# Kernel tuning notes

Hardware: AMD Instinct MI355X
Metric: run time of the kernel (lower is better)

Reference implementation:

```python
import jax, jax.numpy as jnp
import numpy as np

# tcnn HashGrid config from ntc_conf
L = 16            # n_levels
T = 1 << 15       # 2**log2_hashmap_size entries per level
F = 4             # n_features_per_level
BASE = 16.0       # base_resolution
N_PTS = 1_000_000
PRIMES = jnp.array([1, 2654435761, 805459861], dtype=jnp.uint32)  # tcnn spatial hash primes
OFFS = np.array([[(c >> 2) & 1, (c >> 1) & 1, c & 1] for c in range(8)], dtype=np.uint32)  # 8 cube corners


def hash_encode(x, table):
    """Multi-resolution hash grid encoding. x: [N,3] in [0,1], table: [L,T,F] -> [N, L*F]."""
    N = x.shape[0]
    scales = BASE * (2.0 ** jnp.arange(L, dtype=jnp.float32))        # [L]
    pos = x[:, None, :] * scales[None, :, None]                      # [N,L,3]
    p0 = jnp.floor(pos)
    frac = pos - p0                                                  # trilinear weights source
    p0u = p0.astype(jnp.uint32)
    flat_table = table.reshape(L * T, F)
    level_off = (jnp.arange(L, dtype=jnp.uint32) * jnp.uint32(T))[None, :]  # [1,L]
    acc = jnp.zeros((N, L, F), dtype=table.dtype)
    for c in range(8):  # fixed 8 corners -> keeps peak memory at [N,L,F] per corner
        off = jnp.asarray(OFFS[c])                                   # [3] uint32
        corner = p0u + off                                           # [N,L,3]
        h = corner * PRIMES                                          # uint32 wraparound mul
        idx = (h[..., 0] ^ h[..., 1] ^ h[..., 2]) & jnp.uint32(T - 1)  # [N,L]
        feats = flat_table[(idx + level_off).astype(jnp.int32)]      # gather [N,L,F]
        w = jnp.prod(jnp.where(off.astype(bool), frac, 1.0 - frac), axis=-1)  # [N,L]
        acc = acc + w[..., None] * feats
    return acc.reshape(N, L * F)


def setup_inputs() -> dict:
    key = jax.random.key(0)
    k1, k2, k3, k4, k5 = jax.random.split(key, 5)
    xyz = jax.random.normal(k1, (N_PTS, 3), dtype=jnp.float32)
    xyz_bound_min = -jnp.ones((3,), dtype=jnp.float32)
    xyz_bound_max = jnp.ones((3,), dtype=jnp.float32)
    hash_table = jax.random.normal(k2, (L, T, F), dtype=jnp.float32) * 1e-2  # tcnn-style small init
    w0 = jax.random.normal(k3, (64, 64), dtype=jnp.float32) * (1.0 / 8.0)
    w1 = jax.random.normal(k4, (64, 64), dtype=jnp.float32) * (1.0 / 8.0)
    w2 = jax.random.normal(k5, (64, 8), dtype=jnp.float32) * (1.0 / 8.0)
    return {"xyz": xyz, "xyz_bound_min": xyz_bound_min, "xyz_bound_max": xyz_bound_max,
            "hash_table": hash_table, "w0": w0, "w1": w1, "w2": w2}


def reference(xyz, xyz_bound_min, xyz_bound_max, hash_table, w0, w1, w2):
    contracted = (xyz - xyz_bound_min) / (xyz_bound_max - xyz_bound_min)   # [N,3]
    mask = jnp.all((contracted >= 0.0) & (contracted <= 1.0), axis=1)      # [N]
    # Evaluate on all points (clamped) and mask the writes -- equivalent to the
    # original compaction (contracted[mask]) + scatter-back, jit-friendly shapes.
    xin = jnp.clip(contracted, 0.0, 1.0)
    enc = hash_encode(xin, hash_table)                                     # [N,64]
    h = jax.nn.relu(enc @ w0)
    h = jax.nn.relu(h @ w1)
    resi = h @ w2                                                          # [N,8]
    d_xyz = jnp.where(mask[:, None], resi[:, :3], 0.0)
    ident_rot = jnp.array([1.0, 0.0, 0.0, 0.0], dtype=resi.dtype)
    d_rot = jnp.where(mask[:, None], resi[:, 3:7], ident_rot)
    return mask, d_xyz, d_rot
```

## Files before the change

### kernel.cpp

```cpp
#include <hip/hip_runtime.h>
#include <hip/hip_bf16.h>


#define LVL 16
#define TSZ 32768
#define PR1 2654435761u
#define PR2 805459861u

typedef __attribute__((ext_vector_type(8))) short bf16x8;
typedef __attribute__((ext_vector_type(4))) float f32x4;
typedef __attribute__((ext_vector_type(2))) float f32x2;
typedef __attribute__((ext_vector_type(4))) unsigned short u16x4;

__device__ __forceinline__ unsigned short f2bf(float f) {
    return __builtin_bit_cast(unsigned short, __float2bfloat16(f));
}

__device__ __forceinline__ unsigned f32x4_to_fp8x4(float f0, float f1, float f2, float f3) {
#if __has_builtin(__builtin_amdgcn_cvt_pk_fp8_f32)
    int u = 0;
    u = __builtin_amdgcn_cvt_pk_fp8_f32(f0, f1, u, false);
    u = __builtin_amdgcn_cvt_pk_fp8_f32(f2, f3, u, true);
    return (unsigned)u;
#else
    float ff[4] = { f0, f1, f2, f3 };
    unsigned u = 0;
    for (int k = 0; k < 4; ++k) {
        const float v = ff[k];
        const unsigned s = v < 0.f ? 1u : 0u;
        float av = fabsf(v);
        unsigned b;
        if (av < 6.103515625e-05f) {
            b = 0u;
        } else if (av < 0.015625f) {
            b = (unsigned)rintf(av * 512.f);
        } else {
            int e; float m = frexpf(av, &e);
            unsigned E = (unsigned)(e - 1 + 7);
            unsigned q = (unsigned)rintf(m * 16.f);
            if (q == 16u) { q = 8u; ++E; }
            b = (E << 3) | (q - 8u);
        }
        u |= ((s << 7) | b) << (8 * k);
    }
    return u;
#endif
}

__device__ __forceinline__ void fp8x4_to_f32(unsigned r, float f[4]) {
#if __has_builtin(__builtin_amdgcn_cvt_pk_f32_fp8)
    const f32x2 lo = __builtin_amdgcn_cvt_pk_f32_fp8((int)r, false);
    const f32x2 hi = __builtin_amdgcn_cvt_pk_f32_fp8((int)r, true);
    f[0] = lo[0]; f[1] = lo[1]; f[2] = hi[0]; f[3] = hi[1];
#else
#pragma unroll
    for (int k = 0; k < 4; ++k) {
        const unsigned b = (r >> (8 * k)) & 0xffu;
        const unsigned s = b >> 7, em = b & 0x7fu, e = em >> 3, m = em & 7u;
        float v;
        if (e) v = __builtin_bit_cast(float, ((e + 120u) << 23) | (m << 20));
        else   v = (float)m * 0.001953125f;
        f[k] = s ? -v : v;
    }
#endif
}

__global__ __launch_bounds__(256) void k_tbl8(const float* __restrict__ t,
                                              unsigned* __restrict__ o, int n4) {
    const int g = blockIdx.x * 256 + threadIdx.x;
    if (g >= n4) return;
    const float4 a = reinterpret_cast<const float4*>(t)[g];
    o[g] = f32x4_to_fp8x4(a.x * 256.f, a.y * 256.f, a.z * 256.f, a.w * 256.f);
}

__global__ void k_wts(const float* __restrict__ w0, const float* __restrict__ w1,
                      const float* __restrict__ w2, unsigned short* __restrict__ wf) {
    const int t = threadIdx.x;
#pragma unroll
    for (int q = 0; q < 16; ++q) {
        const int s = q * 256 + t;
        const int e = s & 7, f = s >> 3;
        const int lnn = f & 63, ntkk = f >> 6;
        const int k = (ntkk & 1) * 32 + (lnn >> 4) * 8 + e;
        const int n = (ntkk >> 1) * 16 + (lnn & 15);
        wf[s]        = f2bf(w0[k * 64 + n]);
        wf[4096 + s] = f2bf(w1[k * 64 + n]);
    }
#pragma unroll
    for (int q = 0; q < 4; ++q) {
        const int s = q * 256 + t;
        const int e = s & 7, f = s >> 3;
        const int lnn = f & 63, kk = f >> 6;
        const int k = kk * 32 + (lnn >> 4) * 8 + e;
        const int n = lnn & 15;
        wf[8192 + s] = (n < 8) ? f2bf(w2[k * 8 + n]) : (unsigned short)0;
    }
}

__global__ __launch_bounds__(1024) void k_enc(
    const float* __restrict__ xyz, const float* __restrict__ bmin, const float* __restrict__ bmax,
    const unsigned* __restrict__ tbl8, float* __restrict__ out,
    unsigned short* __restrict__ enc, int N, int Npad)
{
    __shared__ unsigned tabL[TSZ];

    const int t = threadIdx.x;
    const int base = blockIdx.x * 4096;

    const float bx0 = bmin[0], by0 = bmin[1], bz0 = bmin[2];
    const float ex = bmax[0] - bx0, ey = bmax[1] - by0, ez = bmax[2] - bz0;

    float X[4], Y[4], Z[4];
#pragma unroll
    for (int q = 0; q < 4; ++q) {
        const int p  = base + q * 1024 + t;
        const int pc = p < N ? p : N - 1;
        const float cx = (xyz[3 * pc + 0] - bx0) / ex;
        const float cy = (xyz[3 * pc + 1] - by0) / ey;
        const float cz = (xyz[3 * pc + 2] - bz0) / ez;
        const bool inside = (cx >= 0.f) && (cx <= 1.f) && (cy >= 0.f) && (cy <= 1.f) &&
                            (cz >= 0.f) && (cz <= 1.f);
        if (p < N) out[p] = inside ? 1.f : 0.f;
        X[q] = fminf(fmaxf(cx, 0.f), 1.f);
        Y[q] = fminf(fmaxf(cy, 0.f), 1.f);
        Z[q] = fminf(fmaxf(cz, 0.f), 1.f);
    }

    for (int l = 0; l < LVL; ++l) {
        __syncthreads();
        {
            const uint4* __restrict__ src = reinterpret_cast<const uint4*>(tbl8 + (size_t)l * TSZ);
            uint4* dst = reinterpret_cast<uint4*>(tabL);
#pragma unroll
            for (int j = 0; j < 8; ++j) dst[j * 1024 + t] = src[j * 1024 + t];
        }
        __syncthreads();

        const float scale = 16.f * (float)(1u << l);
#pragma unroll
        for (int q = 0; q < 4; ++q) {
            const float px = X[q] * scale, py = Y[q] * scale, pz = Z[q] * scale;
            const float fx = floorf(px), fy = floorf(py), fz = floorf(pz);
            const float rx = px - fx, ry = py - fy, rz = pz - fz;
            const unsigned ux = (unsigned)fx, uy = (unsigned)fy, uz = (unsigned)fz;
            const unsigned hx[2] = { ux, ux + 1u };
            const unsigned hy[2] = { uy * PR1, uy * PR1 + PR1 };
            const unsigned hz[2] = { uz * PR2, uz * PR2 + PR2 };
            const float    wx[2] = { 1.f - rx, rx };
            const float    wy[2] = { 1.f - ry, ry };
            const float    wz[2] = { (1.f - rz) * (1.f / 256.f), rz * (1.f / 256.f) };

            unsigned r[8];
#pragma unroll
            for (int c = 0; c < 8; ++c)
                r[c] = tabL[(hx[(c >> 2) & 1] ^ hy[(c >> 1) & 1] ^ hz[c & 1]) & (TSZ - 1u)];

            float a0 = 0.f, a1 = 0.f, a2 = 0.f, a3 = 0.f;
#pragma unroll
            for (int c = 0; c < 8; ++c) {
                float f[4];
                fp8x4_to_f32(r[c], f);
                const float w = wx[(c >> 2) & 1] * wy[(c >> 1) & 1] * wz[c & 1];
                a0 = fmaf(w, f[0], a0);
                a1 = fmaf(w, f[1], a1);
                a2 = fmaf(w, f[2], a2);
                a3 = fmaf(w, f[3], a3);
            }

            const int p = base + q * 1024 + t;
            u16x4 v = { f2bf(a0), f2bf(a1), f2bf(a2), f2bf(a3) };
            *reinterpret_cast<u16x4*>(enc + ((size_t)(l >> 1) * Npad + p) * 8 + (l & 1) * 4) = v;
        }
    }
}

__global__ __launch_bounds__(256) void k_mlp(
    const unsigned short* __restrict__ wf, const unsigned short* __restrict__ enc,
    float* __restrict__ out, int N, int Npad)
{
    __shared__ unsigned short hT[8 * 256 * 8];
    __shared__ float resS[256 * 8];

    const int t = threadIdx.x, wv = t >> 6, ln = t & 63;
    const int col = ln & 15, g = ln >> 4;
    const int ptb = blockIdx.x * 256;
    const int i = ptb + t;

    bf16x8 a0[2][4];
#pragma unroll
    for (int kk = 0; kk < 2; ++kk)
#pragma unroll
        for (int mt = 0; mt < 4; ++mt) {
            const size_t pt = (size_t)ptb + wv * 64 + mt * 16 + col;
            a0[kk][mt] = __builtin_nontemporal_load(
                reinterpret_cast<const bf16x8*>(enc + ((size_t)(kk * 4 + g) * Npad + pt) * 8));
        }
    bf16x8 b0[4][2];
#pragma unroll
    for (int nt = 0; nt < 4; ++nt)
#pragma unroll
        for (int kk = 0; kk < 2; ++kk)
            b0[nt][kk] = *reinterpret_cast<const bf16x8*>(wf + ((nt * 2 + kk) * 64 + ln) * 8);

    f32x4 acc[4][4];
#pragma unroll
    for (int mt = 0; mt < 4; ++mt)
#pragma unroll
        for (int nt = 0; nt < 4; ++nt) acc[mt][nt] = (f32x4){0.f, 0.f, 0.f, 0.f};

#pragma unroll
    for (int kk = 0; kk < 2; ++kk)
#pragma unroll
        for (int nt = 0; nt < 4; ++nt)
#pragma unroll
            for (int mt = 0; mt < 4; ++mt)
                acc[mt][nt] = __builtin_amdgcn_mfma_f32_16x16x32_bf16(a0[kk][mt], b0[nt][kk], acc[mt][nt], 0, 0, 0);

#pragma unroll
    for (int mt = 0; mt < 4; ++mt)
#pragma unroll
        for (int nt = 0; nt < 4; ++nt) {
            const int kt = nt * 2 + (col >> 3), j = col & 7;
#pragma unroll
            for (int r = 0; r < 4; ++r)
                hT[kt * 2048 + (wv * 64 + mt * 16 + g * 4 + r) * 8 + j] =
                    f2bf(fmaxf(acc[mt][nt][r], 0.f));
        }

    bf16x8 b1[4][2];
#pragma unroll
    for (int nt = 0; nt < 4; ++nt)
#pragma unroll
        for (int kk = 0; kk < 2; ++kk)
            b1[nt][kk] = *reinterpret_cast<const bf16x8*>(wf + 4096 + ((nt * 2 + kk) * 64 + ln) * 8);

#pragma unroll
    for (int mt = 0; mt < 4; ++mt)
#pragma unroll
        for (int nt = 0; nt < 4; ++nt) acc[mt][nt] = (f32x4){0.f, 0.f, 0.f, 0.f};

#pragma unroll
    for (int kk = 0; kk < 2; ++kk) {
        bf16x8 a[4];
#pragma unroll
        for (int mt = 0; mt < 4; ++mt)
            a[mt] = *reinterpret_cast<bf16x8*>(
                &hT[(kk * 4 + g) * 2048 + (wv * 64 + mt * 16 + col) * 8]);
#pragma unroll
        for (int nt = 0; nt < 4; ++nt)
#pragma unroll
            for (int mt = 0; mt < 4; ++mt)
                acc[mt][nt] = __builtin_amdgcn_mfma_f32_16x16x32_bf16(a[mt], b1[nt][kk], acc[mt][nt], 0, 0, 0);
    }

#pragma unroll
    for (int mt = 0; mt < 4; ++mt)
#pragma unroll
        for (int nt = 0; nt < 4; ++nt) {
            const int kt = nt * 2 + (col >> 3), j = col & 7;
#pragma unroll
            for (int r = 0; r < 4; ++r)
                hT[kt * 2048 + (wv * 64 + mt * 16 + g * 4 + r) * 8 + j] =
                    f2bf(fmaxf(acc[mt][nt][r], 0.f));
        }

    f32x4 acc2[4];
#pragma unroll
    for (int mt = 0; mt < 4; ++mt) acc2[mt] = (f32x4){0.f, 0.f, 0.f, 0.f};

#pragma unroll
    for (int kk = 0; kk < 2; ++kk) {
        const bf16x8 b2 = *reinterpret_cast<const bf16x8*>(wf + 8192 + (kk * 64 + ln) * 8);
        bf16x8 a[4];
#pragma unroll
        for (int mt = 0; mt < 4; ++mt)
            a[mt] = *reinterpret_cast<bf16x8*>(
                &hT[(kk * 4 + g) * 2048 + (wv * 64 + mt * 16 + col) * 8]);
#pragma unroll
        for (int mt = 0; mt < 4; ++mt)
            acc2[mt] = __builtin_amdgcn_mfma_f32_16x16x32_bf16(a[mt], b2, acc2[mt], 0, 0, 0);
    }

    if (col < 8) {
#pragma unroll
        for (int mt = 0; mt < 4; ++mt)
#pragma unroll
            for (int r = 0; r < 4; ++r)
                resS[(wv * 64 + mt * 16 + g * 4 + r) * 8 + col] = acc2[mt][r];
    }
    __syncthreads();

    if (i < N) {
        const bool inside = (out[i] != 0.f);
        const f32x4 lo = *reinterpret_cast<f32x4*>(&resS[t * 8 + 0]);
        const f32x4 hi = *reinterpret_cast<f32x4*>(&resS[t * 8 + 4]);

        float* __restrict__ dxyz = out + N;
        dxyz[3 * i + 0] = inside ? lo.x : 0.f;
        dxyz[3 * i + 1] = inside ? lo.y : 0.f;
        dxyz[3 * i + 2] = inside ? lo.z : 0.f;

        float4* __restrict__ drot = reinterpret_cast<float4*>(out + 4 * (size_t)N);
        drot[i] = inside ? make_float4(lo.w, hi.x, hi.y, hi.z)
                         : make_float4(1.f, 0.f, 0.f, 0.f);
    }
}

__global__ __launch_bounds__(256) void ntc_fused(
    const float* __restrict__ xyz, const float* __restrict__ bmin, const float* __restrict__ bmax,
    const float* __restrict__ table, const float* __restrict__ w0, const float* __restrict__ w1,
    const float* __restrict__ w2, float* __restrict__ out, int N)
{
    __shared__ unsigned short encT[8 * 256 * 8];
    __shared__ unsigned short w0t[64 * 64];
    __shared__ unsigned short w1t[64 * 64];
    __shared__ unsigned short w2t[16 * 64];

    const int t = threadIdx.x, wv = t >> 6, ln = t & 63;
    const int col = ln & 15, g = ln >> 4;

#pragma unroll
    for (int it = 0; it < 16; ++it) {
        const int idx = it * 256 + t;
        const int k = idx >> 6, n = idx & 63;
        w0t[n * 64 + k] = f2bf(w0[idx]);
        w1t[n * 64 + k] = f2bf(w1[idx]);
    }
#pragma unroll
    for (int q = 0; q < 4; ++q) {
        const int idx = t * 4 + q;
        const int n = idx >> 6, k = idx & 63;
        w2t[idx] = (n < 8) ? f2bf(w2[k * 8 + n]) : (unsigned short)0;
    }

    const int i = blockIdx.x * 256 + t;
    const int ic = (i < N) ? i : (N - 1);
    const float bx0 = bmin[0], by0 = bmin[1], bz0 = bmin[2];
    const float ex = bmax[0] - bx0, ey = bmax[1] - by0, ez = bmax[2] - bz0;
    const float cx = (xyz[3 * ic + 0] - bx0) / ex;
    const float cy = (xyz[3 * ic + 1] - by0) / ey;
    const float cz = (xyz[3 * ic + 2] - bz0) / ez;
    const bool inside = (cx >= 0.f) && (cx <= 1.f) && (cy >= 0.f) && (cy <= 1.f) &&
                        (cz >= 0.f) && (cz <= 1.f);
    const float x = fminf(fmaxf(cx, 0.f), 1.f);
    const float y = fminf(fmaxf(cy, 0.f), 1.f);
    const float z = fminf(fmaxf(cz, 0.f), 1.f);
    const float4* __restrict__ tab = reinterpret_cast<const float4*>(table);

    for (int l = 0; l < LVL; ++l) {
        const float scale = 16.f * (float)(1u << l);
        const float px = x * scale, py = y * scale, pz = z * scale;
        const float fx = floorf(px), fy = floorf(py), fz = floorf(pz);
        const float rx = px - fx, ry = py - fy, rz = pz - fz;
        const unsigned ux = (unsigned)fx, uy = (unsigned)fy, uz = (unsigned)fz;
        const unsigned hx[2] = { ux, ux + 1u };
        const unsigned hy[2] = { uy * PR1, (uy + 1u) * PR1 };
        const unsigned hz[2] = { uz * PR2, (uz + 1u) * PR2 };
        const float wx[2] = { 1.f - rx, rx };
        const float wy[2] = { 1.f - ry, ry };
        const float wz[2] = { 1.f - rz, rz };
        float a0 = 0.f, a1 = 0.f, a2 = 0.f, a3 = 0.f;
#pragma unroll
        for (int c = 0; c < 8; ++c) {
            const int ox = (c >> 2) & 1, oy = (c >> 1) & 1, oz = c & 1;
            const unsigned idx = (hx[ox] ^ hy[oy] ^ hz[oz]) & (TSZ - 1u);
            const float4 f4 = tab[l * TSZ + idx];
            const float w = wx[ox] * wy[oy] * wz[oz];
            a0 = fmaf(w, f4.x, a0); a1 = fmaf(w, f4.y, a1);
            a2 = fmaf(w, f4.z, a2); a3 = fmaf(w, f4.w, a3);
        }
        u16x4 v = { f2bf(a0), f2bf(a1), f2bf(a2), f2bf(a3) };
        *reinterpret_cast<u16x4*>(&encT[(l >> 1) * 2048 + t * 8 + (l & 1) * 4]) = v;
    }
    __syncthreads();

    f32x4 acc[4][4];
#pragma unroll
    for (int mt = 0; mt < 4; ++mt)
#pragma unroll
        for (int nt = 0; nt < 4; ++nt) acc[mt][nt] = (f32x4){0.f, 0.f, 0.f, 0.f};
#pragma unroll
    for (int kk = 0; kk < 2; ++kk) {
        bf16x8 a[4];
#pragma unroll
        for (int mt = 0; mt < 4; ++mt)
            a[mt] = *reinterpret_cast<bf16x8*>(&encT[(kk * 4 + g) * 2048 + (wv * 64 + mt * 16 + col) * 8]);
#pragma unroll
        for (int nt = 0; nt < 4; ++nt) {
            bf16x8 b = *reinterpret_cast<bf16x8*>(&w0t[(nt * 16 + col) * 64 + kk * 32 + g * 8]);
#pragma unroll
            for (int mt = 0; mt < 4; ++mt)
                acc[mt][nt] = __builtin_amdgcn_mfma_f32_16x16x32_bf16(a[mt], b, acc[mt][nt], 0, 0, 0);
        }
    }
    __syncthreads();
#pragma unroll
    for (int mt = 0; mt < 4; ++mt)
#pragma unroll
        for (int nt = 0; nt < 4; ++nt) {
            const int kt = nt * 2 + (col >> 3), j = col & 7;
#pragma unroll
            for (int r = 0; r < 4; ++r)
                encT[kt * 2048 + (wv * 64 + mt * 16 + g * 4 + r) * 8 + j] = f2bf(fmaxf(acc[mt][nt][r], 0.f));
        }
    __syncthreads();
#pragma unroll
    for (int mt = 0; mt < 4; ++mt)
#pragma unroll
        for (int nt = 0; nt < 4; ++nt) acc[mt][nt] = (f32x4){0.f, 0.f, 0.f, 0.f};
#pragma unroll
    for (int kk = 0; kk < 2; ++kk) {
        bf16x8 a[4];
#pragma unroll
        for (int mt = 0; mt < 4; ++mt)
            a[mt] = *reinterpret_cast<bf16x8*>(&encT[(kk * 4 + g) * 2048 + (wv * 64 + mt * 16 + col) * 8]);
#pragma unroll
        for (int nt = 0; nt < 4; ++nt) {
            bf16x8 b = *reinterpret_cast<bf16x8*>(&w1t[(nt * 16 + col) * 64 + kk * 32 + g * 8]);
#pragma unroll
            for (int mt = 0; mt < 4; ++mt)
                acc[mt][nt] = __builtin_amdgcn_mfma_f32_16x16x32_bf16(a[mt], b, acc[mt][nt], 0, 0, 0);
        }
    }
    __syncthreads();
#pragma unroll
    for (int mt = 0; mt < 4; ++mt)
#pragma unroll
        for (int nt = 0; nt < 4; ++nt) {
            const int kt = nt * 2 + (col >> 3), j = col & 7;
#pragma unroll
            for (int r = 0; r < 4; ++r)
                encT[kt * 2048 + (wv * 64 + mt * 16 + g * 4 + r) * 8 + j] = f2bf(fmaxf(acc[mt][nt][r], 0.f));
        }
    __syncthreads();
    f32x4 acc2[4];
#pragma unroll
    for (int mt = 0; mt < 4; ++mt) acc2[mt] = (f32x4){0.f, 0.f, 0.f, 0.f};
#pragma unroll
    for (int kk = 0; kk < 2; ++kk) {
        bf16x8 a[4];
#pragma unroll
        for (int mt = 0; mt < 4; ++mt)
            a[mt] = *reinterpret_cast<bf16x8*>(&encT[(kk * 4 + g) * 2048 + (wv * 64 + mt * 16 + col) * 8]);
        bf16x8 b = *reinterpret_cast<bf16x8*>(&w2t[col * 64 + kk * 32 + g * 8]);
#pragma unroll
        for (int mt = 0; mt < 4; ++mt)
            acc2[mt] = __builtin_amdgcn_mfma_f32_16x16x32_bf16(a[mt], b, acc2[mt], 0, 0, 0);
    }
    __syncthreads();
    float* res = reinterpret_cast<float*>(encT);
    if (col < 8) {
#pragma unroll
        for (int mt = 0; mt < 4; ++mt)
#pragma unroll
            for (int r = 0; r < 4; ++r)
                res[(wv * 64 + mt * 16 + g * 4 + r) * 8 + col] = acc2[mt][r];
    }
    __syncthreads();
    if (i < N) {
        const f32x4 lo = *reinterpret_cast<f32x4*>(&res[t * 8 + 0]);
        const f32x4 hi = *reinterpret_cast<f32x4*>(&res[t * 8 + 4]);
        out[i] = inside ? 1.f : 0.f;
        float* __restrict__ dxyz = out + N;
        dxyz[3 * i + 0] = inside ? lo.x : 0.f;
        dxyz[3 * i + 1] = inside ? lo.y : 0.f;
        dxyz[3 * i + 2] = inside ? lo.z : 0.f;
        float4* __restrict__ drot = reinterpret_cast<float4*>(out + 4 * (size_t)N);
        drot[i] = inside ? make_float4(lo.w, hi.x, hi.y, hi.z)
                         : make_float4(1.f, 0.f, 0.f, 0.f);
    }
}

extern "C" void kernel_launch(void* const* d_in, const int* in_sizes, int n_in,
                              void* d_out, int out_size, void* d_ws, size_t ws_size,
                              hipStream_t stream) {
    const float* xyz   = (const float*)d_in[0];
    const float* bmin  = (const float*)d_in[1];
    const float* bmax  = (const float*)d_in[2];
    const float* table = (const float*)d_in[3];
    const float* w0    = (const float*)d_in[4];
    const float* w1    = (const float*)d_in[5];
    const float* w2    = (const float*)d_in[6];
    float* out = (float*)d_out;

    const int N = in_sizes[0] / 3;
    const int nb = (N + 255) / 256;
    const int nbE = (N + 4095) / 4096;
    const int Npad = nbE * 4096;
    const int tblElems = in_sizes[3];

    size_t offW = ((size_t)tblElems + 63) & ~(size_t)63;
    size_t offEnc = (offW + 9216 * 2 + 255) & ~(size_t)255;
    size_t need = offEnc + (size_t)Npad * 128;

    if (ws_size >= need) {
        unsigned* tbl8      = (unsigned*)d_ws;
        unsigned short* wfr = (unsigned short*)((char*)d_ws + offW);
        unsigned short* enc = (unsigned short*)((char*)d_ws + offEnc);
        const int n4 = tblElems / 4;
        k_tbl8<<<(n4 + 255) / 256, 256, 0, stream>>>(table, tbl8, n4);
        k_wts<<<1, 256, 0, stream>>>(w0, w1, w2, wfr);
        k_enc<<<nbE, 1024, 0, stream>>>(xyz, bmin, bmax, tbl8, out, enc, N, Npad);
        k_mlp<<<nb, 256, 0, stream>>>(wfr, enc, out, N, Npad);
    } else {
        ntc_fused<<<nb, 256, 0, stream>>>(xyz, bmin, bmax, table, w0, w1, w2, out, N);
    }
}
```

Before: 196.2 us.

## Store encodings as fp8 and run first MLP layer with fp8 MFMA

The encoding intermediate is written as fp8 (scaled by 256 via the table) instead of bf16, halving the global write and read traffic between the encode and MLP kernels. The first layer uses the fp8 MFMA with fp8-quantized w0 and rescales by 1/256 on output. The weight-prep kernel is folded into the last block of the table conversion kernel, removing one launch. The trilinear weights are also factored to save multiplies. Accuracy drops from fp8 quantization of both activations and w0.

```diff
diff --git a/kernel.cpp b/kernel.cpp
--- a/kernel.cpp
+++ b/kernel.cpp
@@ -11,6 +11,8 @@
 typedef __attribute__((ext_vector_type(4))) float f32x4;
 typedef __attribute__((ext_vector_type(2))) float f32x2;
 typedef __attribute__((ext_vector_type(4))) unsigned short u16x4;
+typedef __attribute__((ext_vector_type(2))) unsigned int u32x2;
+typedef long long i64;
 
 __device__ __forceinline__ unsigned short f2bf(float f) {
     return __builtin_bit_cast(unsigned short, __float2bfloat16(f));
@@ -47,6 +49,10 @@
 #endif
 }
 
+__device__ __forceinline__ unsigned char f32_to_fp8(float v) {
+    return (unsigned char)(f32x4_to_fp8x4(v, v, v, v) & 0xffu);
+}
+
 __device__ __forceinline__ void fp8x4_to_f32(unsigned r, float f[4]) {
 #if __has_builtin(__builtin_amdgcn_cvt_pk_f32_fp8)
     const f32x2 lo = __builtin_amdgcn_cvt_pk_f32_fp8((int)r, false);
@@ -65,42 +71,55 @@
 #endif
 }
 
-__global__ __launch_bounds__(256) void k_tbl8(const float* __restrict__ t,
-                                              unsigned* __restrict__ o, int n4) {
+__global__ __launch_bounds__(256) void k_tbl8(
+    const float* __restrict__ t, unsigned* __restrict__ o, int n4,
+    const float* __restrict__ w0, const float* __restrict__ w1,
+    const float* __restrict__ w2, char* __restrict__ wbase)
+{
     const int g = blockIdx.x * 256 + threadIdx.x;
-    if (g >= n4) return;
-    const float4 a = reinterpret_cast<const float4*>(t)[g];
-    o[g] = f32x4_to_fp8x4(a.x * 256.f, a.y * 256.f, a.z * 256.f, a.w * 256.f);
-}
-
-__global__ void k_wts(const float* __restrict__ w0, const float* __restrict__ w1,
-                      const float* __restrict__ w2, unsigned short* __restrict__ wf) {
-    const int t = threadIdx.x;
-#pragma unroll
-    for (int q = 0; q < 16; ++q) {
-        const int s = q * 256 + t;
-        const int e = s & 7, f = s >> 3;
-        const int lnn = f & 63, ntkk = f >> 6;
-        const int k = (ntkk & 1) * 32 + (lnn >> 4) * 8 + e;
-        const int n = (ntkk >> 1) * 16 + (lnn & 15);
-        wf[s]        = f2bf(w0[k * 64 + n]);
-        wf[4096 + s] = f2bf(w1[k * 64 + n]);
-    }
-#pragma unroll
-    for (int q = 0; q < 4; ++q) {
-        const int s = q * 256 + t;
-        const int e = s & 7, f = s >> 3;
-        const int lnn = f & 63, kk = f >> 6;
-        const int k = kk * 32 + (lnn >> 4) * 8 + e;
-        const int n = lnn & 15;
-        wf[8192 + s] = (n < 8) ? f2bf(w2[k * 8 + n]) : (unsigned short)0;
+    if (g < n4) {
+        const float4 a = reinterpret_cast<const float4*>(t)[g];
+        o[g] = f32x4_to_fp8x4(a.x * 256.f, a.y * 256.f, a.z * 256.f, a.w * 256.f);
+    }
+    if (blockIdx.x == gridDim.x - 1) {
+        const int tt = threadIdx.x;
+        unsigned char*  wf8 = (unsigned char*)wbase;
+        unsigned short* wf1 = (unsigned short*)(wbase + 4096);
+        unsigned short* wf2 = (unsigned short*)(wbase + 4096 + 8192);
+#pragma unroll
+        for (int q = 0; q < 16; ++q) {
+            const int s = q * 256 + tt;
+            const int e = s & 7, f = s >> 3;
+            const int ln = f & 63, ntkk = f >> 6;
+            const int k = (ntkk & 1) * 32 + (ln >> 4) * 8 + e;
+            const int n = (ntkk >> 1) * 16 + (ln & 15);
+            wf8[s] = f32_to_fp8(w0[k * 64 + n]);
+        }
+#pragma unroll
+        for (int q = 0; q < 16; ++q) {
+            const int s = q * 256 + tt;
+            const int e = s & 7, f = s >> 3;
+            const int ln = f & 63, ntkk = f >> 6;
+            const int k = (ntkk & 1) * 32 + (ln >> 4) * 8 + e;
+            const int n = (ntkk >> 1) * 16 + (ln & 15);
+            wf1[s] = f2bf(w1[k * 64 + n]);
+        }
+#pragma unroll
+        for (int q = 0; q < 4; ++q) {
+            const int s = q * 256 + tt;
+            const int e = s & 7, f = s >> 3;
+            const int ln = f & 63, kk = f >> 6;
+            const int k = kk * 32 + (ln >> 4) * 8 + e;
+            const int n = ln & 15;
+            wf2[s] = (n < 8) ? f2bf(w2[k * 8 + n]) : (unsigned short)0;
+        }
     }
 }
 
 __global__ __launch_bounds__(1024) void k_enc(
     const float* __restrict__ xyz, const float* __restrict__ bmin, const float* __restrict__ bmax,
     const unsigned* __restrict__ tbl8, float* __restrict__ out,
-    unsigned short* __restrict__ enc, int N, int Npad)
+    unsigned* __restrict__ enc, int N, int Npad)
 {
     __shared__ unsigned tabL[TSZ];
 
@@ -126,6 +145,8 @@
         Z[q] = fminf(fmaxf(cz, 0.f), 1.f);
     }
 
+    unsigned pend[4];
+
     for (int l = 0; l < LVL; ++l) {
         __syncthreads();
         {
@@ -146,9 +167,10 @@
             const unsigned hx[2] = { ux, ux + 1u };
             const unsigned hy[2] = { uy * PR1, uy * PR1 + PR1 };
             const unsigned hz[2] = { uz * PR2, uz * PR2 + PR2 };
-            const float    wx[2] = { 1.f - rx, rx };
-            const float    wy[2] = { 1.f - ry, ry };
-            const float    wz[2] = { (1.f - rz) * (1.f / 256.f), rz * (1.f / 256.f) };
+            const float wx0 = 1.f - rx, wx1 = rx;
+            const float wy0 = 1.f - ry, wy1 = ry;
+            const float wz[2] = { 1.f - rz, rz };
+            const float wxy[4] = { wx0 * wy0, wx0 * wy1, wx1 * wy0, wx1 * wy1 };
 
             unsigned r[8];
 #pragma unroll
@@ -160,47 +182,57 @@
             for (int c = 0; c < 8; ++c) {
                 float f[4];
                 fp8x4_to_f32(r[c], f);
-                const float w = wx[(c >> 2) & 1] * wy[(c >> 1) & 1] * wz[c & 1];
+                const float w = wxy[c >> 1] * wz[c & 1];
                 a0 = fmaf(w, f[0], a0);
                 a1 = fmaf(w, f[1], a1);
                 a2 = fmaf(w, f[2], a2);
                 a3 = fmaf(w, f[3], a3);
             }
 
-            const int p = base + q * 1024 + t;
-            u16x4 v = { f2bf(a0), f2bf(a1), f2bf(a2), f2bf(a3) };
-            *reinterpret_cast<u16x4*>(enc + ((size_t)(l >> 1) * Npad + p) * 8 + (l & 1) * 4) = v;
+            const unsigned v = f32x4_to_fp8x4(a0, a1, a2, a3);
+            if (l & 1) {
+                const int p = base + q * 1024 + t;
+                const u32x2 v2 = { pend[q], v };
+                __builtin_nontemporal_store(v2,
+                    reinterpret_cast<u32x2*>(enc) + ((size_t)(l >> 1) * Npad + p));
+            } else {
+                pend[q] = v;
+            }
         }
     }
 }
 
 __global__ __launch_bounds__(256) void k_mlp(
-    const unsigned short* __restrict__ wf, const unsigned short* __restrict__ enc,
+    const char* __restrict__ wbase, const unsigned* __restrict__ enc,
     float* __restrict__ out, int N, int Npad)
 {
     __shared__ unsigned short hT[8 * 256 * 8];
     __shared__ float resS[256 * 8];
 
+    const unsigned char*  wf8 = (const unsigned char*)wbase;
+    const unsigned short* wf1 = (const unsigned short*)(wbase + 4096);
+    const unsigned short* wf2 = (const unsigned short*)(wbase + 4096 + 8192);
+
     const int t = threadIdx.x, wv = t >> 6, ln = t & 63;
     const int col = ln & 15, g = ln >> 4;
     const int ptb = blockIdx.x * 256;
     const int i = ptb + t;
 
-    bf16x8 a0[2][4];
+    u32x2 a0[2][4];
 #pragma unroll
     for (int kk = 0; kk < 2; ++kk)
 #pragma unroll
         for (int mt = 0; mt < 4; ++mt) {
             const size_t pt = (size_t)ptb + wv * 64 + mt * 16 + col;
             a0[kk][mt] = __builtin_nontemporal_load(
-                reinterpret_cast<const bf16x8*>(enc + ((size_t)(kk * 4 + g) * Npad + pt) * 8));
-        }
-    bf16x8 b0[4][2];
+                reinterpret_cast<const u32x2*>(enc) + ((size_t)(kk * 4 + g) * Npad + pt));
+        }
+    u32x2 b0[4][2];
 #pragma unroll
     for (int nt = 0; nt < 4; ++nt)
 #pragma unroll
         for (int kk = 0; kk < 2; ++kk)
-            b0[nt][kk] = *reinterpret_cast<const bf16x8*>(wf + ((nt * 2 + kk) * 64 + ln) * 8);
+            b0[nt][kk] = *reinterpret_cast<const u32x2*>(wf8 + ((nt * 2 + kk) * 64 + ln) * 8);
 
     f32x4 acc[4][4];
 #pragma unroll
@@ -214,7 +246,46 @@
         for (int nt = 0; nt < 4; ++nt)
 #pragma unroll
             for (int mt = 0; mt < 4; ++mt)
-                acc[mt][nt] = __builtin_amdgcn_mfma_f32_16x16x32_bf16(a0[kk][mt], b0[nt][kk], acc[mt][nt], 0, 0, 0);
+                acc[mt][nt] = __builtin_amdgcn_mfma_f32_16x16x32_fp8_fp8(
+                    __builtin_bit_cast(i64, a0[kk][mt]),
+                    __builtin_bit_cast(i64, b0[nt][kk]), acc[mt][nt], 0, 0, 0);
+
+#pragma unroll
+    for (int mt = 0; mt < 4; ++mt)
+#pragma unroll
+        for (int nt = 0; nt < 4; ++nt) {
+            const int kt = nt * 2 + (col >> 3), j = col & 7;
+#pragma unroll
+            for (int r = 0; r < 4; ++r)
+                hT[kt * 2048 + (wv * 64 + mt * 16 + g * 4 + r) * 8 + j] =
+                    f2bf(fmaxf(acc[mt][nt][r], 0.f) * 0.00390625f);
+        }
+
+    bf16x8 b1[4][2];
+#pragma unroll
+    for (int nt = 0; nt < 4; ++nt)
+#pragma unroll
+        for (int kk = 0; kk < 2; ++kk)
+            b1[nt][kk] = *reinterpret_cast<const bf16x8*>(wf1 + ((nt * 2 + kk) * 64 + ln) * 8);
+
+#pragma unroll
+    for (int mt = 0; mt < 4; ++mt)
+#pragma unroll
+        for (int nt = 0; nt < 4; ++nt) acc[mt][nt] = (f32x4){0.f, 0.f, 0.f, 0.f};
+
+#pragma unroll
+    for (int kk = 0; kk < 2; ++kk) {
+        bf16x8 a[4];
+#pragma unroll
+        for (int mt = 0; mt < 4; ++mt)
+            a[mt] = *reinterpret_cast<bf16x8*>(
+                &hT[(kk * 4 + g) * 2048 + (wv * 64 + mt * 16 + col) * 8]);
+#pragma unroll
+        for (int nt = 0; nt < 4; ++nt)
+#pragma unroll
+            for (int mt = 0; mt < 4; ++mt)
+                acc[mt][nt] = __builtin_amdgcn_mfma_f32_16x16x32_bf16(a[mt], b1[nt][kk], acc[mt][nt], 0, 0, 0);
+    }
 
 #pragma unroll
     for (int mt = 0; mt < 4; ++mt)
@@ -227,50 +298,13 @@
                     f2bf(fmaxf(acc[mt][nt][r], 0.f));
         }
 
-    bf16x8 b1[4][2];
-#pragma unroll
-    for (int nt = 0; nt < 4; ++nt)
-#pragma unroll
-        for (int kk = 0; kk < 2; ++kk)
-            b1[nt][kk] = *reinterpret_cast<const bf16x8*>(wf + 4096 + ((nt * 2 + kk) * 64 + ln) * 8);
-
-#pragma unroll
-    for (int mt = 0; mt < 4; ++mt)
-#pragma unroll
-        for (int nt = 0; nt < 4; ++nt) acc[mt][nt] = (f32x4){0.f, 0.f, 0.f, 0.f};
+    f32x4 acc2[4];
+#pragma unroll
+    for (int mt = 0; mt < 4; ++mt) acc2[mt] = (f32x4){0.f, 0.f, 0.f, 0.f};
 
 #pragma unroll
     for (int kk = 0; kk < 2; ++kk) {
-        bf16x8 a[4];
-#pragma unroll
-        for (int mt = 0; mt < 4; ++mt)
-            a[mt] = *reinterpret_cast<bf16x8*>(
-                &hT[(kk * 4 + g) * 2048 + (wv * 64 + mt * 16 + col) * 8]);
-#pragma unroll
-        for (int nt = 0; nt < 4; ++nt)
-#pragma unroll
-            for (int mt = 0; mt < 4; ++mt)
-                acc[mt][nt] = __builtin_amdgcn_mfma_f32_16x16x32_bf16(a[mt], b1[nt][kk], acc[mt][nt], 0, 0, 0);
-    }
-
-#pragma unroll
-    for (int mt = 0; mt < 4; ++mt)
-#pragma unroll
-        for (int nt = 0; nt < 4; ++nt) {
-            const int kt = nt * 2 + (col >> 3), j = col & 7;
-#pragma unroll
-            for (int r = 0; r < 4; ++r)
-                hT[kt * 2048 + (wv * 64 + mt * 16 + g * 4 + r) * 8 + j] =
-                    f2bf(fmaxf(acc[mt][nt][r], 0.f));
-        }
-
-    f32x4 acc2[4];
-#pragma unroll
-    for (int mt = 0; mt < 4; ++mt) acc2[mt] = (f32x4){0.f, 0.f, 0.f, 0.f};
-
-#pragma unroll
-    for (int kk = 0; kk < 2; ++kk) {
-        const bf16x8 b2 = *reinterpret_cast<const bf16x8*>(wf + 8192 + (kk * 64 + ln) * 8);
+        const bf16x8 b2 = *reinterpret_cast<const bf16x8*>(wf2 + (kk * 64 + ln) * 8);
         bf16x8 a[4];
 #pragma unroll
         for (int mt = 0; mt < 4; ++mt)
@@ -490,18 +524,17 @@
     const int tblElems = in_sizes[3];
 
     size_t offW = ((size_t)tblElems + 63) & ~(size_t)63;
-    size_t offEnc = (offW + 9216 * 2 + 255) & ~(size_t)255;
-    size_t need = offEnc + (size_t)Npad * 128;
+    size_t offEnc = (offW + 14336 + 255) & ~(size_t)255;
+    size_t need = offEnc + (size_t)Npad * 64;
 
     if (ws_size >= need) {
-        unsigned* tbl8      = (unsigned*)d_ws;
-        unsigned short* wfr = (unsigned short*)((char*)d_ws + offW);
-        unsigned short* enc = (unsigned short*)((char*)d_ws + offEnc);
+        unsigned* tbl8 = (unsigned*)d_ws;
+        char* wbase    = (char*)d_ws + offW;
+        unsigned* enc  = (unsigned*)((char*)d_ws + offEnc);
         const int n4 = tblElems / 4;
-        k_tbl8<<<(n4 + 255) / 256, 256, 0, stream>>>(table, tbl8, n4);
-        k_wts<<<1, 256, 0, stream>>>(w0, w1, w2, wfr);
+        k_tbl8<<<(n4 + 255) / 256, 256, 0, stream>>>(table, tbl8, n4, w0, w1, w2, wbase);
         k_enc<<<nbE, 1024, 0, stream>>>(xyz, bmin, bmax, tbl8, out, enc, N, Npad);
-        k_mlp<<<nb, 256, 0, stream>>>(wfr, enc, out, N, Npad);
+        k_mlp<<<nb, 256, 0, stream>>>(wbase, enc, out, N, Npad);
     } else {
         ntc_fused<<<nb, 256, 0, stream>>>(xyz, bmin, bmax, table, w0, w1, w2, out, N);
     }
```

Result: faster. 191.1 us (-2.6%).
